# Optimization experiments

Measured on AMD Instinct MI355X. Metric: run time of the kernel, lower is better.

Reference implementation:

```python
import jax, jax.numpy as jnp
import numpy as np

N, C, H, W = 8, 64, 256, 256
HO, WO = 256, 256


def setup_inputs() -> dict:
    key = jax.random.key(0)
    kx, kg = jax.random.split(key)
    x = jax.random.normal(kx, (N, C, H, W), dtype=jnp.float32)
    # normalized sampling coords in [-1, 1], last dim = (x, y)
    grid = jax.random.uniform(kg, (N, HO, WO, 2), dtype=jnp.float32, minval=-1.0, maxval=1.0)
    return {"x": x, "grid": grid}


def reference(x, grid):
    # Bilinear grid sample, align_corners=True, border-clamped indices
    # x: [N, C, H, W]; grid: [N, Ho, Wo, 2] in [-1, 1]
    n, c, h, w = x.shape
    ix = (grid[..., 0] + 1.0) * 0.5 * (w - 1)  # [N, Ho, Wo] unnormalized x coord
    iy = (grid[..., 1] + 1.0) * 0.5 * (h - 1)

    x0f = jnp.floor(ix)
    y0f = jnp.floor(iy)
    wx1 = ix - x0f  # frac weights
    wy1 = iy - y0f
    wx0 = 1.0 - wx1
    wy0 = 1.0 - wy1

    x0 = jnp.clip(x0f, 0, w - 1).astype(jnp.int32)
    x1 = jnp.clip(x0f + 1.0, 0, w - 1).astype(jnp.int32)
    y0 = jnp.clip(y0f, 0, h - 1).astype(jnp.int32)
    y1 = jnp.clip(y0f + 1.0, 0, h - 1).astype(jnp.int32)

    xt = jnp.transpose(x, (0, 2, 3, 1))  # [N, H, W, C] for channels-last gather
    b = jnp.arange(n)[:, None, None]  # [N, 1, 1] batch index

    def gather(yi, xi):
        return xt[b, yi, xi]  # [N, Ho, Wo, C]

    out = (gather(y0, x0) * (wy0 * wx0)[..., None]
           + gather(y0, x1) * (wy0 * wx1)[..., None]
           + gather(y1, x0) * (wy1 * wx0)[..., None]
           + gather(y1, x1) * (wy1 * wx1)[..., None])
    return jnp.transpose(out, (0, 3, 1, 2))  # [N, C, Ho, Wo]
```

## Files before the change

### kernel.cpp

```cpp
#include <hip/hip_runtime.h>
#include <hip/hip_bf16.h>


constexpr int N = 8, C = 64, H = 256, W = 256, HO = 256, WO = 256;
constexpr int NPIX = N * HO * WO;
constexpr int PLANE = H * W;
constexpr size_t XT_BYTES = (size_t)N * PLANE * C * sizeof(unsigned short);

typedef unsigned short ushortv8 __attribute__((ext_vector_type(8)));

__device__ __forceinline__ float bf16_to_f(unsigned short u) {
  union { unsigned int i; float f; } v;
  v.i = ((unsigned int)u) << 16;
  return v.f;
}

__global__ __launch_bounds__(256) void transpose_kernel(
    const float* __restrict__ x, unsigned int* __restrict__ xt) {
  __shared__ float tile[64][65];
  int tx = threadIdx.x;
  int ty = threadIdx.y;
  int t = (ty << 6) + tx;
  int tileIdx = blockIdx.x;
  int n = tileIdx >> 10;
  int pixb = (tileIdx & 1023) << 6;

  const float* xn = x + (size_t)n * C * PLANE;
#pragma unroll
  for (int k = 0; k < 16; ++k) {
    int c = (k << 2) + ty;
    tile[c][tx] = __builtin_nontemporal_load(&xn[(size_t)c * PLANE + pixb + tx]);
  }
  __syncthreads();

  unsigned int* xtw = xt + ((size_t)(n * PLANE + pixb)) * 32;
  int chp = t & 31;
#pragma unroll
  for (int k = 0; k < 8; ++k) {
    int p = (k << 3) + (t >> 5);
    float f0 = tile[2 * chp][p];
    float f1 = tile[2 * chp + 1][p];
    __hip_bfloat162 h2 = __float22bfloat162_rn(make_float2(f0, f1));
    unsigned int w;
    __builtin_memcpy(&w, &h2, 4);
    xtw[(size_t)p * 32 + chp] = w;
  }
}

__global__ __launch_bounds__(64) void sample_kernel(
    const unsigned short* __restrict__ xt, const float* __restrict__ grid,
    float* __restrict__ out) {
  __shared__ float tile[64][33];
  __shared__ float4 wts[64];
  __shared__ int bs[64];

  int lane = threadIdx.x;
  int pixb = blockIdx.x << 6;
  int p_idx = pixb + lane;
  int n = p_idx >> 16;

  float2 g = ((const float2*)grid)[p_idx];
  float ix = (g.x + 1.0f) * 0.5f * (float)(W - 1);
  float iy = (g.y + 1.0f) * 0.5f * (float)(H - 1);
  float x0f = floorf(ix), y0f = floorf(iy);
  float fx = ix - x0f, fy = iy - y0f;
  float cx0 = fminf(fmaxf(x0f,        0.f), (float)(W - 1));
  float cx1 = fminf(fmaxf(x0f + 1.f,  0.f), (float)(W - 1));
  float cy0 = fminf(fmaxf(y0f,        0.f), (float)(H - 1));
  float cy1 = fminf(fmaxf(y0f + 1.f,  0.f), (float)(H - 1));
  int x0 = (int)cx0, x1 = (int)cx1, y0 = (int)cy0, y1 = (int)cy1;
  int xl = min(x0, W - 2), yl = min(y0, H - 2);
  float wx0 = 1.f - fx, wx1 = fx, wy0 = 1.f - fy, wy1 = fy;
  float wxl = (x0 == xl ? wx0 : 0.f) + (x1 == xl ? wx1 : 0.f);
  float wxh = (x0 == xl + 1 ? wx0 : 0.f) + (x1 == xl + 1 ? wx1 : 0.f);
  float wyl = (y0 == yl ? wy0 : 0.f) + (y1 == yl ? wy1 : 0.f);
  float wyh = (y0 == yl + 1 ? wy0 : 0.f) + (y1 == yl + 1 ? wy1 : 0.f);
  wts[lane] = make_float4(wyl * wxl, wyl * wxh, wyh * wxl, wyh * wxh);
  bs[lane] = ((n << 16) | (yl << 8) | xl) << 6;
  __syncthreads();

  int prow = pixb & (PLANE - 1);
  float* outn = out + (size_t)n * C * PLANE + prow;

  int ps    = lane >> 3;
  int chunk = lane & 7;

  for (int h = 0; h < 2; ++h) {
#pragma unroll
    for (int i = 0; i < 4; ++i) {
      int ph = (i << 3) + ps;
      int p  = (h << 5) + ph;
      float4 wv = wts[p];
      const ushortv8* src =
          (const ushortv8*)(xt + bs[p] + (chunk << 3));
      ushortv8 a  = src[0];
      ushortv8 b  = src[C / 8];
      ushortv8 cv = src[(C * W) / 8];
      ushortv8 d  = src[(C * W + C) / 8];
#pragma unroll
      for (int j = 0; j < 8; ++j) {
        float r = bf16_to_f(a[j])  * wv.x + bf16_to_f(b[j]) * wv.y
                + bf16_to_f(cv[j]) * wv.z + bf16_to_f(d[j]) * wv.w;
        tile[(chunk << 3) + j][ph] = r;
      }
    }
    __syncthreads();
    int pq = lane & 31;
    int cb = lane >> 5;
#pragma unroll 8
    for (int k = 0; k < 32; ++k) {
      int c = (k << 1) + cb;
      __builtin_nontemporal_store(tile[c][pq],
                                  &outn[(size_t)c * PLANE + (h << 5) + pq]);
    }
    __syncthreads();
  }
}

__global__ __launch_bounds__(256) void grid_sample_fallback(
    const float* __restrict__ x, const float* __restrict__ grid,
    float* __restrict__ out) {
  int idx = blockIdx.x * blockDim.x + threadIdx.x;
  if (idx >= NPIX) return;
  int wo = idx & (WO - 1);
  int ho = (idx >> 8) & (HO - 1);
  int n  = idx >> 16;
  float2 g = ((const float2*)grid)[idx];
  float ix = (g.x + 1.0f) * 0.5f * (float)(W - 1);
  float iy = (g.y + 1.0f) * 0.5f * (float)(H - 1);
  float x0f = floorf(ix), y0f = floorf(iy);
  float wx1 = ix - x0f, wy1 = iy - y0f;
  float wx0 = 1.0f - wx1, wy0 = 1.0f - wy1;
  int x0 = (int)fminf(fmaxf(x0f,        0.0f), (float)(W - 1));
  int x1 = (int)fminf(fmaxf(x0f + 1.0f, 0.0f), (float)(W - 1));
  int y0 = (int)fminf(fmaxf(y0f,        0.0f), (float)(H - 1));
  int y1 = (int)fminf(fmaxf(y0f + 1.0f, 0.0f), (float)(H - 1));
  float w00 = wy0 * wx0, w01 = wy0 * wx1, w10 = wy1 * wx0, w11 = wy1 * wx1;
  int o00 = y0 * W + x0, o01 = y0 * W + x1, o10 = y1 * W + x0, o11 = y1 * W + x1;
  const float* xn = x + (size_t)n * C * PLANE;
  float* on = out + (size_t)n * C * PLANE + (size_t)ho * WO + wo;
#pragma unroll 4
  for (int c = 0; c < C; ++c) {
    const float* xc = xn + c * PLANE;
    float v = xc[o00] * w00 + xc[o01] * w01 + xc[o10] * w10 + xc[o11] * w11;
    __builtin_nontemporal_store(v, on + (size_t)c * PLANE);
  }
}

extern "C" void kernel_launch(void* const* d_in, const int* in_sizes, int n_in,
                              void* d_out, int out_size, void* d_ws, size_t ws_size,
                              hipStream_t stream) {
  const float* x    = (const float*)d_in[0];
  const float* grid = (const float*)d_in[1];
  float* out        = (float*)d_out;

  if (ws_size >= XT_BYTES) {
    transpose_kernel<<<N * PLANE / 64, dim3(64, 4), 0, stream>>>(
        x, (unsigned int*)d_ws);
    sample_kernel<<<NPIX / 64, 64, 0, stream>>>(
        (const unsigned short*)d_ws, grid, out);
  } else {
    grid_sample_fallback<<<NPIX / 256, 256, 0, stream>>>(x, grid, out);
  }
}
```

Before: 262.3 us.

## Software-pipeline bf16 gathers with per-wave tiles and shuffle-broadcast weights

The sampling kernel now runs 256-thread blocks in which each wave owns its own shared tile. Per-pixel weights and base offsets are broadcast with wave shuffles instead of going through shared memory, which removes all block barriers. Gathers are issued two groups ahead through a three-slot register ring, so loads overlap the bf16 unpack and FMA work. Output is written with 16-byte nontemporal vector stores. The cost is higher register pressure from the in-flight slots, and the vector reads from the 33-float-stride shared tile are not 16-byte aligned.

```diff
diff --git a/kernel.cpp b/kernel.cpp
--- a/kernel.cpp
+++ b/kernel.cpp
@@ -8,6 +8,7 @@
 constexpr size_t XT_BYTES = (size_t)N * PLANE * C * sizeof(unsigned short);
 
 typedef unsigned short ushortv8 __attribute__((ext_vector_type(8)));
+typedef float floatx4 __attribute__((ext_vector_type(4)));
 
 __device__ __forceinline__ float bf16_to_f(unsigned short u) {
   union { unsigned int i; float f; } v;
@@ -47,15 +48,15 @@
   }
 }
 
-__global__ __launch_bounds__(64) void sample_kernel(
+__global__ __launch_bounds__(256, 4) void sample_kernel(
     const unsigned short* __restrict__ xt, const float* __restrict__ grid,
     float* __restrict__ out) {
-  __shared__ float tile[64][33];
-  __shared__ float4 wts[64];
-  __shared__ int bs[64];
+  __shared__ float tile[4][64][33];
 
-  int lane = threadIdx.x;
-  int pixb = blockIdx.x << 6;
+  int tid  = threadIdx.x;
+  int wid  = tid >> 6;
+  int lane = tid & 63;
+  int pixb = (blockIdx.x << 8) + (wid << 6);
   int p_idx = pixb + lane;
   int n = p_idx >> 16;
 
@@ -75,46 +76,76 @@
   float wxh = (x0 == xl + 1 ? wx0 : 0.f) + (x1 == xl + 1 ? wx1 : 0.f);
   float wyl = (y0 == yl ? wy0 : 0.f) + (y1 == yl ? wy1 : 0.f);
   float wyh = (y0 == yl + 1 ? wy0 : 0.f) + (y1 == yl + 1 ? wy1 : 0.f);
-  wts[lane] = make_float4(wyl * wxl, wyl * wxh, wyh * wxl, wyh * wxh);
-  bs[lane] = ((n << 16) | (yl << 8) | xl) << 6;
-  __syncthreads();
+  float w00 = wyl * wxl, w01 = wyl * wxh, w10 = wyh * wxl, w11 = wyh * wxh;
+  int bs = ((n << 16) | (yl << 8) | xl) << 6;
+
+  int ps    = lane >> 3;
+  int chunk = lane & 7;
+  const unsigned short* xtc = xt + (chunk << 3);
+  float (*tl)[33] = tile[wid];
 
   int prow = pixb & (PLANE - 1);
   float* outn = out + (size_t)n * C * PLANE + prow;
 
-  int ps    = lane >> 3;
-  int chunk = lane & 7;
+  ushortv8 A[3][4];
 
-  for (int h = 0; h < 2; ++h) {
+#define ISSUE(gg, slot)                                                        \
+  {                                                                            \
+    int p = ((gg) << 3) + ps;                                                  \
+    int bsp = __shfl(bs, p);                                                   \
+    const ushortv8* src = (const ushortv8*)(xtc + bsp);                        \
+    A[slot][0] = src[0];                                                       \
+    A[slot][1] = src[C / 8];                                                   \
+    A[slot][2] = src[(C * W) / 8];                                             \
+    A[slot][3] = src[(C * W + C) / 8];                                         \
+  }
+
+  ISSUE(0, 0)
+  ISSUE(1, 1)
+
 #pragma unroll
-    for (int i = 0; i < 4; ++i) {
-      int ph = (i << 3) + ps;
-      int p  = (h << 5) + ph;
-      float4 wv = wts[p];
-      const ushortv8* src =
-          (const ushortv8*)(xt + bs[p] + (chunk << 3));
-      ushortv8 a  = src[0];
-      ushortv8 b  = src[C / 8];
-      ushortv8 cv = src[(C * W) / 8];
-      ushortv8 d  = src[(C * W + C) / 8];
+  for (int gq = 0; gq < 8; ++gq) {
+    if (gq + 2 < 8) {
+      const int sl = (gq + 2) % 3;
+      ISSUE(gq + 2, sl)
+    }
+    {
+      const int sl = gq % 3;
+      int p = (gq << 3) + ps;
+      float wa = __shfl(w00, p), wb = __shfl(w01, p);
+      float wc = __shfl(w10, p), wd = __shfl(w11, p);
+      int ph = ((gq & 3) << 3) + ps;
 #pragma unroll
-      for (int j = 0; j < 8; ++j) {
-        float r = bf16_to_f(a[j])  * wv.x + bf16_to_f(b[j]) * wv.y
-                + bf16_to_f(cv[j]) * wv.z + bf16_to_f(d[j]) * wv.w;
-        tile[(chunk << 3) + j][ph] = r;
+      for (int jp = 0; jp < 4; ++jp) {
+        unsigned int ua = ((unsigned int*)&A[sl][0])[jp];
+        unsigned int ub = ((unsigned int*)&A[sl][1])[jp];
+        unsigned int uc = ((unsigned int*)&A[sl][2])[jp];
+        unsigned int ud = ((unsigned int*)&A[sl][3])[jp];
+        float a0 = __uint_as_float(ua << 16), a1 = __uint_as_float(ua & 0xffff0000u);
+        float b0 = __uint_as_float(ub << 16), b1 = __uint_as_float(ub & 0xffff0000u);
+        float c0 = __uint_as_float(uc << 16), c1 = __uint_as_float(uc & 0xffff0000u);
+        float d0 = __uint_as_float(ud << 16), d1 = __uint_as_float(ud & 0xffff0000u);
+        float r0 = a0 * wa + b0 * wb + c0 * wc + d0 * wd;
+        float r1 = a1 * wa + b1 * wb + c1 * wc + d1 * wd;
+        int ch = (chunk << 3) + (jp << 1);
+        tl[ch][ph]     = r0;
+        tl[ch + 1][ph] = r1;
       }
     }
-    __syncthreads();
-    int pq = lane & 31;
-    int cb = lane >> 5;
-#pragma unroll 8
-    for (int k = 0; k < 32; ++k) {
-      int c = (k << 1) + cb;
-      __builtin_nontemporal_store(tile[c][pq],
-                                  &outn[(size_t)c * PLANE + (h << 5) + pq]);
+    if ((gq & 3) == 3) {
+      int h = gq >> 2;
+      int cs = lane >> 3;
+      int q  = lane & 7;
+#pragma unroll
+      for (int k = 0; k < 8; ++k) {
+        int c = (k << 3) + cs;
+        floatx4 v = *(floatx4*)&tl[c][q << 2];
+        __builtin_nontemporal_store(
+            v, (floatx4*)(outn + (size_t)c * PLANE + (h << 5) + (q << 2)));
+      }
     }
-    __syncthreads();
   }
+#undef ISSUE
 }
 
 __global__ __launch_bounds__(256) void grid_sample_fallback(
@@ -157,7 +188,7 @@
   if (ws_size >= XT_BYTES) {
     transpose_kernel<<<N * PLANE / 64, dim3(64, 4), 0, stream>>>(
         x, (unsigned int*)d_ws);
-    sample_kernel<<<NPIX / 64, 64, 0, stream>>>(
+    sample_kernel<<<NPIX / 256, 256, 0, stream>>>(
         (const unsigned short*)d_ws, grid, out);
   } else {
     grid_sample_fallback<<<NPIX / 256, 256, 0, stream>>>(x, grid, out);
```

Result: no change. 263.5 us (+0.4%).
